# Kernel optimization log

Hardware: AMD Instinct MI355X
Metric: run time of the kernel (lower is better)

Reference implementation:

```python
import jax, jax.numpy as jnp
import numpy as np
import math

EMB_DIM = 2048
HEAD_NUMS = 16
HEAD_DIM = EMB_DIM // HEAD_NUMS


def setup_inputs() -> dict:
    key = jax.random.key(0)
    k1, k2, k3, k4, k5 = jax.random.split(key, 5)
    B, S = 2, 2048
    X = jax.random.normal(k1, (B, S, EMB_DIM), dtype=jnp.float32)
    mask = jnp.ones((B, S), dtype=jnp.int32)
    # torch nn.Linear weights: [out_features, in_features]
    W_qkv = jax.random.normal(k2, (3 * EMB_DIM, EMB_DIM), dtype=jnp.float32) / math.sqrt(EMB_DIM)
    b_qkv = jax.random.normal(k3, (3 * EMB_DIM,), dtype=jnp.float32) * 0.01
    W_o = jax.random.normal(k4, (EMB_DIM, EMB_DIM), dtype=jnp.float32) / math.sqrt(EMB_DIM)
    b_o = jax.random.normal(k5, (EMB_DIM,), dtype=jnp.float32) * 0.01
    return {"X": X, "mask": mask, "W_qkv": W_qkv, "b_qkv": b_qkv, "W_o": W_o, "b_o": b_o}


def _rope_tables(seq_len):
    # Bug-faithful to source: exponent divides by full emb_dim, not head_dim.
    angle = 1.0 / jnp.power(10000.0, jnp.arange(0, HEAD_DIM, 2, dtype=jnp.float32) / EMB_DIM)
    t = jnp.arange(seq_len, dtype=jnp.float32)
    freqs = t[:, None] * angle[None, :]            # [S, HEAD_DIM//2]
    freqs = jnp.repeat(freqs, 2, axis=-1)          # [S, HEAD_DIM] (repeat_interleave)
    return jnp.cos(freqs), jnp.sin(freqs)


def _trans(x):
    # de-interleave pairs, then concat([-odd, even]) along last dim (as in source)
    B, H, S, D = x.shape
    xr = x.reshape(B, H, S, D // 2, 2)
    x1, x2 = xr[..., 0], xr[..., 1]
    return jnp.concatenate([-x2, x1], axis=-1)


def reference(X, mask, W_qkv, b_qkv, W_o, b_o):
    B, S, E = X.shape
    cos, sin = _rope_tables(S)                      # [S, HEAD_DIM]
    qkv = X @ W_qkv.T + b_qkv                       # [B, S, 3E]
    qkv = qkv.reshape(B, S, 3, HEAD_NUMS, HEAD_DIM).transpose(2, 0, 3, 1, 4)
    Q, K, V = qkv[0], qkv[1], qkv[2]                # [B, H, S, D]
    c = cos[None, None, :, :]
    s = sin[None, None, :, :]
    Q = c * Q + s * _trans(Q)
    K = c * K + s * _trans(K)
    scores = jnp.einsum('bhqd,bhkd->bhqk', Q, K) / math.sqrt(HEAD_DIM)
    pad = mask[:, None, None, :]                    # [B,1,1,S]
    scores = jnp.where(pad == 0, -1e9, scores)
    attn = jax.nn.softmax(scores, axis=-1)          # dropout = identity (eval)
    out = jnp.einsum('bhqk,bhkd->bhqd', attn, V)    # [B,H,S,D]
    out = out.transpose(0, 2, 1, 3).reshape(B, S, E)
    return out @ W_o.T + b_o
```

## Files before the change

### kernel.cpp

```cpp
#include <hip/hip_runtime.h>
#include <hip/hip_bf16.h>
#include <math.h>

typedef __bf16 bf16x8 __attribute__((ext_vector_type(8)));
typedef float  f32x4  __attribute__((ext_vector_type(4)));
typedef float  f32x16 __attribute__((ext_vector_type(16)));
typedef unsigned short ushort_t;
typedef ushort_t us4 __attribute__((ext_vector_type(4)));

#define MFMA16(a, b, c) __builtin_amdgcn_mfma_f32_16x16x32_bf16((a), (b), (c), 0, 0, 0)
#define MFMA32(a, b, c) __builtin_amdgcn_mfma_f32_32x32x16_bf16((a), (b), (c), 0, 0, 0)

__device__ __forceinline__ float bf2f(ushort_t h) {
    union { unsigned u; float f; } v; v.u = ((unsigned)h) << 16; return v.f;
}
__device__ __forceinline__ ushort_t f2bf(float x) {
    union { float f; unsigned u; } v; v.f = x;
    unsigned r = v.u + 0x7FFFu + ((v.u >> 16) & 1u);
    return (ushort_t)(r >> 16);
}
__device__ __forceinline__ void gl2lds16(const void* g, void* l) {
    __builtin_amdgcn_global_load_lds((__attribute__((address_space(1))) void*)(g),
                                     (__attribute__((address_space(3))) void*)(l),
                                     16, 0, 0);
}

__global__ __launch_bounds__(256) void detect_kernel(const ushort_t* __restrict__ w, int* flag)
{
    __shared__ int cnt[256];
    const int t = threadIdx.x;
    int c = 0;
    for (int i = t; i < 65536; i += 256) {
        const unsigned hw = w[i];
        const unsigned e = (hw >> 7) & 0xFFu;
        if (e == 0xFFu || (e == 0u && (hw & 0x7Fu) != 0u)) c++;
    }
    cnt[t] = c;
    __syncthreads();
    for (int s = 128; s > 0; s >>= 1) {
        if (t < s) cnt[t] += cnt[t + s];
        __syncthreads();
    }
    if (t == 0) flag[0] = (cnt[0] >= 8) ? 1 : 0;
}

__global__ __launch_bounds__(256) void convert_kernel(const void* __restrict__ src,
                                                      ushort_t* __restrict__ dst,
                                                      int n, const int* __restrict__ flag)
{
    const int i0 = (blockIdx.x * 256 + threadIdx.x) * 8;
    if (i0 + 8 > n) return;
    if (flag[0]) {
        const f32x4 a = *(const f32x4*)((const float*)src + i0);
        const f32x4 b = *(const f32x4*)((const float*)src + i0 + 4);
        ushort_t o[8];
        o[0]=f2bf(a[0]); o[1]=f2bf(a[1]); o[2]=f2bf(a[2]); o[3]=f2bf(a[3]);
        o[4]=f2bf(b[0]); o[5]=f2bf(b[1]); o[6]=f2bf(b[2]); o[7]=f2bf(b[3]);
        *(bf16x8*)(dst + i0) = *(const bf16x8*)o;
    } else {
        *(bf16x8*)(dst + i0) = *(const bf16x8*)((const ushort_t*)src + i0);
    }
}

__global__ __launch_bounds__(512, 2) void gemm256_bt_bias(
    const ushort_t* __restrict__ A, const ushort_t* __restrict__ B,
    const ushort_t* __restrict__ bias, ushort_t* __restrict__ C,
    int M, int N, int K)
{
    __shared__ __align__(16) ushort_t SM[65536];
    const int tid = threadIdx.x;
    const int l = tid & 63, ln = l & 15, q2 = l >> 4;
    const int w = tid >> 6, wm = w >> 2, wn = w & 3;
    const int m0 = blockIdx.y * 256, n0 = blockIdx.x * 256;
    const int NT = K >> 6;

#define STG_A256(slot, kbase, o) do { \
    const int s_ = (o) * 512 + tid; const int r_ = s_ >> 2; \
    const int q_ = (s_ & 3) ^ ((r_ >> 1) & 3); \
    gl2lds16(A + (size_t)(m0 + r_) * K + (kbase) + q_ * 8, \
             SM + (slot) * 16384 + s_ * 8); } while (0)
#define STG_B256(slot, kbase, o) do { \
    const int s_ = (o) * 512 + tid; const int r_ = s_ >> 2; \
    const int q_ = (s_ & 3) ^ ((r_ >> 1) & 3); \
    gl2lds16(B + (size_t)(n0 + r_) * K + (kbase) + q_ * 8, \
             SM + (slot) * 16384 + 8192 + s_ * 8); } while (0)
#define DSA256(slot, row) (*(const bf16x8*)(SM + (slot) * 16384 + (row) * 32 + ((q2 ^ (((row) >> 1) & 3)) << 3)))
#define DSB256(slot, row) (*(const bf16x8*)(SM + (slot) * 16384 + 8192 + (row) * 32 + ((q2 ^ (((row) >> 1) & 3)) << 3)))
#define BAR256() asm volatile("s_barrier" ::: "memory")

    f32x4 acc[8][4];
    const f32x4 z4 = {0.f, 0.f, 0.f, 0.f};
#pragma unroll
    for (int i = 0; i < 8; i++)
#pragma unroll
        for (int j = 0; j < 4; j++) acc[i][j] = z4;

    STG_A256(0, 0, 0);  STG_A256(0, 0, 1);  STG_B256(0, 0, 0);  STG_B256(0, 0, 1);
    STG_A256(1, 32, 0); STG_A256(1, 32, 1); STG_B256(1, 32, 0); STG_B256(1, 32, 1);
    if (NT > 1) STG_A256(2, 64, 0);
    asm volatile("s_waitcnt vmcnt(5)" ::: "memory");
    BAR256();

    for (int t = 0; t < NT; ++t) {
        const int s0 = (2 * t) & 3, s1 = (2 * t + 1) & 3;
        const int sA = (2 * t + 2) & 3, sB = (2 * t + 3) & 3;
        const int kA = (t + 1) << 6, kB = kA + 32, kC = (t + 2) << 6;
        const bool stAB = (t < NT - 1), stC = (t < NT - 2);
        const int rA0 = wm * 128, rA1 = wm * 128 + 64, rB = wn * 64;
        bf16x8 a0[4], a1[4], b00[2], b01[2], b10[2], b11[2];

#pragma unroll
        for (int ii = 0; ii < 4; ii++) a0[ii] = DSA256(s0, rA0 + ii * 16 + ln);
        b00[0] = DSB256(s0, rB + ln);
        b00[1] = DSB256(s0, rB + 16 + ln);
        if (stAB) STG_A256(sA, kA, 1);
        __builtin_amdgcn_s_setprio(1);
#pragma unroll
        for (int ii = 0; ii < 4; ii++) {
            acc[ii][0] = MFMA16(a0[ii], b00[0], acc[ii][0]);
            acc[ii][1] = MFMA16(a0[ii], b00[1], acc[ii][1]);
        }
        __builtin_amdgcn_s_setprio(0);
        if (stAB) { asm volatile("s_waitcnt vmcnt(2)" ::: "memory"); }
        else      { asm volatile("s_waitcnt vmcnt(0)" ::: "memory"); }
        BAR256();

#pragma unroll
        for (int ii = 0; ii < 4; ii++) a1[ii] = DSA256(s1, rA0 + ii * 16 + ln);
        b01[0] = DSB256(s1, rB + ln);
        b01[1] = DSB256(s1, rB + 16 + ln);
        if (stAB) STG_B256(sA, kA, 0);
        __builtin_amdgcn_s_setprio(1);
#pragma unroll
        for (int ii = 0; ii < 4; ii++) {
            acc[ii][0] = MFMA16(a1[ii], b01[0], acc[ii][0]);
            acc[ii][1] = MFMA16(a1[ii], b01[1], acc[ii][1]);
        }
        __builtin_amdgcn_s_setprio(0);
        BAR256();

        b10[0] = DSB256(s0, rB + 32 + ln);
        b10[1] = DSB256(s0, rB + 48 + ln);
        if (stAB) STG_B256(sA, kA, 1);
        __builtin_amdgcn_s_setprio(1);
#pragma unroll
        for (int ii = 0; ii < 4; ii++) {
            acc[ii][2] = MFMA16(a0[ii], b10[0], acc[ii][2]);
            acc[ii][3] = MFMA16(a0[ii], b10[1], acc[ii][3]);
        }
        __builtin_amdgcn_s_setprio(0);
        BAR256();

        b11[0] = DSB256(s1, rB + 32 + ln);
        b11[1] = DSB256(s1, rB + 48 + ln);
        if (stAB) STG_A256(sB, kB, 0);
        __builtin_amdgcn_s_setprio(1);
#pragma unroll
        for (int ii = 0; ii < 4; ii++) {
            acc[ii][2] = MFMA16(a1[ii], b11[0], acc[ii][2]);
            acc[ii][3] = MFMA16(a1[ii], b11[1], acc[ii][3]);
        }
        __builtin_amdgcn_s_setprio(0);
        BAR256();

#pragma unroll
        for (int ii = 0; ii < 4; ii++) a0[ii] = DSA256(s0, rA1 + ii * 16 + ln);
        if (stAB) STG_A256(sB, kB, 1);
        __builtin_amdgcn_s_setprio(1);
#pragma unroll
        for (int ii = 0; ii < 4; ii++) {
            acc[4 + ii][2] = MFMA16(a0[ii], b10[0], acc[4 + ii][2]);
            acc[4 + ii][3] = MFMA16(a0[ii], b10[1], acc[4 + ii][3]);
        }
        __builtin_amdgcn_s_setprio(0);
        BAR256();

#pragma unroll
        for (int ii = 0; ii < 4; ii++) a1[ii] = DSA256(s1, rA1 + ii * 16 + ln);
        if (stAB) STG_B256(sB, kB, 0);
        __builtin_amdgcn_s_setprio(1);
#pragma unroll
        for (int ii = 0; ii < 4; ii++) {
            acc[4 + ii][2] = MFMA16(a1[ii], b11[0], acc[4 + ii][2]);
            acc[4 + ii][3] = MFMA16(a1[ii], b11[1], acc[4 + ii][3]);
        }
        __builtin_amdgcn_s_setprio(0);
        BAR256();

        if (stAB) STG_B256(sB, kB, 1);
        __builtin_amdgcn_s_setprio(1);
#pragma unroll
        for (int ii = 0; ii < 4; ii++) {
            acc[4 + ii][0] = MFMA16(a0[ii], b00[0], acc[4 + ii][0]);
            acc[4 + ii][1] = MFMA16(a0[ii], b00[1], acc[4 + ii][1]);
        }
        __builtin_amdgcn_s_setprio(0);
        BAR256();

        if (stC) STG_A256(s0, kC, 0);
        __builtin_amdgcn_s_setprio(1);
#pragma unroll
        for (int ii = 0; ii < 4; ii++) {
            acc[4 + ii][0] = MFMA16(a1[ii], b01[0], acc[4 + ii][0]);
            acc[4 + ii][1] = MFMA16(a1[ii], b01[1], acc[4 + ii][1]);
        }
        __builtin_amdgcn_s_setprio(0);
        if (t < NT - 2)       { asm volatile("s_waitcnt vmcnt(5)" ::: "memory"); }
        else if (t == NT - 2) { asm volatile("s_waitcnt vmcnt(4)" ::: "memory"); }
        BAR256();
    }

#pragma unroll
    for (int j = 0; j < 4; j++) {
        const int n = n0 + wn * 64 + j * 16 + ln;
        const float bv = bf2f(bias[n]);
#pragma unroll
        for (int i = 0; i < 8; i++) {
            const int mrow = m0 + wm * 128 + i * 16 + q2 * 4;
#pragma unroll
            for (int r = 0; r < 4; r++)
                C[(size_t)(mrow + r) * N + n] = f2bf(acc[i][j][r] + bv);
        }
    }
#undef STG_A256
#undef STG_B256
#undef DSA256
#undef DSB256
#undef BAR256
}

__global__ __launch_bounds__(256) void gemm_bt_bias_out(
    const ushort_t* __restrict__ A, const ushort_t* __restrict__ B,
    const ushort_t* __restrict__ bias, void* __restrict__ C,
    int M, int N, int K, const int* __restrict__ flag)
{
    __shared__ __align__(16) ushort_t As[128 * 32];
    __shared__ __align__(16) ushort_t Bs[128 * 32];
    const int tid = threadIdx.x;
    const int w = tid >> 6, l = tid & 63, q = l >> 4, ln = l & 15;
    const int wm = w >> 1, wn = w & 1;
    const int m0 = blockIdx.y * 128, n0 = blockIdx.x * 128;
    const int sr = tid >> 2;
    const int sc = (tid & 3) * 8;

    f32x4 acc[4][4];
    const f32x4 z4 = {0.f, 0.f, 0.f, 0.f};
    for (int i = 0; i < 4; i++) for (int j = 0; j < 4; j++) acc[i][j] = z4;

    for (int k0 = 0; k0 < K; k0 += 32) {
        __syncthreads();
        gl2lds16(A + (size_t)(m0 + sr) * K + k0 + sc,       As + sr * 32 + sc);
        gl2lds16(A + (size_t)(m0 + 64 + sr) * K + k0 + sc,  As + (64 + sr) * 32 + sc);
        gl2lds16(B + (size_t)(n0 + sr) * K + k0 + sc,       Bs + sr * 32 + sc);
        gl2lds16(B + (size_t)(n0 + 64 + sr) * K + k0 + sc,  Bs + (64 + sr) * 32 + sc);
        __syncthreads();
        bf16x8 a[4], bb[4];
        for (int i = 0; i < 4; i++)
            a[i]  = *(const bf16x8*)(As + (wm * 64 + i * 16 + ln) * 32 + q * 8);
        for (int j = 0; j < 4; j++)
            bb[j] = *(const bf16x8*)(Bs + (wn * 64 + j * 16 + ln) * 32 + q * 8);
        for (int i = 0; i < 4; i++)
            for (int j = 0; j < 4; j++)
                acc[i][j] = MFMA16(a[i], bb[j], acc[i][j]);
    }
    const int f = flag[0];
    for (int j = 0; j < 4; j++) {
        const int n = n0 + wn * 64 + j * 16 + ln;
        const float bv = bf2f(bias[n]);
        for (int i = 0; i < 4; i++) {
            const int mrow = m0 + wm * 64 + i * 16 + q * 4;
            for (int r = 0; r < 4; r++) {
                const float val = acc[i][j][r] + bv;
                const size_t idx = (size_t)(mrow + r) * N + n;
                if (f) ((float*)C)[idx] = val;
                else   ((ushort_t*)C)[idx] = f2bf(val);
            }
        }
    }
}

__global__ __launch_bounds__(256) void rope_kernel(ushort_t* qkv)
{
    const int bs = blockIdx.x;
    const int s = bs & 2047;
    const int t = threadIdx.x;
    const size_t base = (size_t)bs * 6144;
    float cv[8], sv[8], qa[8], qp[8], ka[8], kp[8];
    for (int u = 0; u < 8; u++) {
        const int e = u * 256 + t;
        const int j = e & 127;
        const int p = (j < 64) ? (2 * j + 1) : (2 * (j - 64));
        const int hb = e - j;
        const float ang = powf(10000.0f, -(float)(2 * (j >> 1)) / 2048.0f);
        sincosf((float)s * ang, &sv[u], &cv[u]);
        qa[u] = bf2f(qkv[base + hb + j]);
        qp[u] = bf2f(qkv[base + hb + p]);
        ka[u] = bf2f(qkv[base + 2048 + hb + j]);
        kp[u] = bf2f(qkv[base + 2048 + hb + p]);
    }
    __syncthreads();
    for (int u = 0; u < 8; u++) {
        const int e = u * 256 + t;
        const int j = e & 127;
        const int hb = e - j;
        const float sg = (j < 64) ? -1.0f : 1.0f;
        qkv[base + hb + j]        = f2bf(cv[u] * qa[u] + sv[u] * sg * qp[u]);
        qkv[base + 2048 + hb + j] = f2bf(cv[u] * ka[u] + sv[u] * sg * kp[u]);
    }
}

__global__ __launch_bounds__(256) void vtrans_kernel(const ushort_t* __restrict__ qkv,
                                                     ushort_t* __restrict__ Vt)
{
    __shared__ ushort_t tile[64][130];
    const int blk = blockIdx.x;
    const int st = blk & 31, h = (blk >> 5) & 15, b = blk >> 9;
    const int t = threadIdx.x;
    for (int i = 0; i < 32; i++) {
        const int e = i * 256 + t;
        const int r = e >> 7, c = e & 127;
        tile[r][c] = qkv[(size_t)(b * 2048 + st * 64 + r) * 6144 + 4096 + h * 128 + c];
    }
    __syncthreads();
    const int d = t >> 1, s0 = (t & 1) * 32;
    const size_t obase = ((size_t)(b * 16 + h) * 128 + d) * 2048 + st * 64 + s0;
    for (int k = 0; k < 32; k++)
        Vt[obase + k] = tile[s0 + k][d];
}

__global__ __launch_bounds__(256) void flash_kernel(
    const ushort_t* __restrict__ qkv, const ushort_t* __restrict__ Vt,
    const int* __restrict__ mask, ushort_t* __restrict__ AO)
{
    __shared__ __align__(16) ushort_t Ks[64 * 136];
    __shared__ __align__(16) ushort_t Vs[128 * 136];
    __shared__ __align__(16) ushort_t Ps[4 * 32 * 72];
    const int t = threadIdx.x;
    const int w = t >> 6, l = t & 63, lq = l & 31, q2 = l >> 5;
    const int qb = blockIdx.x * 128, h = blockIdx.y, b = blockIdx.z;
    const size_t brow = (size_t)b * 2048;
    const float scale = 0.08838834764831845f;
    const int qrow = qb + w * 32 + lq;

    bf16x8 qf[8];
#pragma unroll
    for (int kb = 0; kb < 8; kb++)
        qf[kb] = *(const bf16x8*)(qkv + (brow + qrow) * 6144 + h * 128 + kb * 16 + q2 * 8);

    float m_old = -1e30f, lsum = 0.f;
    f32x16 acc_o[4];
#pragma unroll
    for (int dt = 0; dt < 4; dt++)
#pragma unroll
        for (int r = 0; r < 16; r++) acc_o[dt][r] = 0.f;

    for (int s0 = 0; s0 < 2048; s0 += 64) {
        const int mk = mask[brow + s0 + l];
        const unsigned long long bm = __ballot(mk != 0);
        __syncthreads();
#pragma unroll
        for (int i = 0; i < 4; i++) {
            const int c = i * 256 + t;
            const int row = c >> 4, cb = c & 15;
            *(bf16x8*)(Ks + row * 136 + cb * 8) =
                *(const bf16x8*)(qkv + (brow + s0 + row) * 6144 + 2048 + h * 128 + cb * 8);
        }
#pragma unroll
        for (int i = 0; i < 4; i++) {
            const int c = i * 256 + t;
            const int row = c >> 3, cb = c & 7;
            *(bf16x8*)(Vs + row * 136 + cb * 8) =
                *(const bf16x8*)(Vt + ((size_t)(b * 16 + h) * 128 + row) * 2048 + s0 + cb * 8);
        }
        __syncthreads();
        f32x16 sa[2];
#pragma unroll
        for (int mt = 0; mt < 2; mt++) {
#pragma unroll
            for (int r = 0; r < 16; r++) sa[mt][r] = 0.f;
#pragma unroll
            for (int kb = 0; kb < 8; kb++) {
                bf16x8 a = *(const bf16x8*)(Ks + (mt * 32 + lq) * 136 + kb * 16 + q2 * 8);
                sa[mt] = MFMA32(a, qf[kb], sa[mt]);
            }
        }
        float p[32];
        float mr = -1e30f;
#pragma unroll
        for (int mt = 0; mt < 2; mt++)
#pragma unroll
            for (int r = 0; r < 16; r++) {
                const int srow = mt * 32 + (r & 3) + 8 * (r >> 2) + 4 * q2;
                const float bias = ((bm >> srow) & 1ull) ? 0.f : -1e9f;
                const float v = sa[mt][r] * scale + bias;
                p[mt * 16 + r] = v;
                mr = fmaxf(mr, v);
            }
        mr = fmaxf(mr, __shfl_xor(mr, 32, 64));
        const float mnew = fmaxf(m_old, mr);
        const float alpha = __expf(m_old - mnew);
        float rs = 0.f;
#pragma unroll
        for (int i = 0; i < 32; i++) { p[i] = __expf(p[i] - mnew); rs += p[i]; }
        rs += __shfl_xor(rs, 32, 64);
        lsum = alpha * lsum + rs;
        m_old = mnew;
#pragma unroll
        for (int dt = 0; dt < 4; dt++)
#pragma unroll
            for (int r = 0; r < 16; r++) acc_o[dt][r] *= alpha;
#pragma unroll
        for (int mt = 0; mt < 2; mt++)
#pragma unroll
            for (int r2 = 0; r2 < 4; r2++) {
                us4 pk;
#pragma unroll
                for (int j = 0; j < 4; j++) pk[j] = f2bf(p[mt * 16 + r2 * 4 + j]);
                *(us4*)(Ps + (w * 32 + lq) * 72 + mt * 32 + r2 * 8 + q2 * 4) = pk;
            }
        bf16x8 pf[4];
#pragma unroll
        for (int kb = 0; kb < 4; kb++)
            pf[kb] = *(const bf16x8*)(Ps + (w * 32 + lq) * 72 + kb * 16 + q2 * 8);
#pragma unroll
        for (int dt = 0; dt < 4; dt++)
#pragma unroll
            for (int kb = 0; kb < 4; kb++) {
                bf16x8 va = *(const bf16x8*)(Vs + (dt * 32 + lq) * 136 + kb * 16 + q2 * 8);
                acc_o[dt] = MFMA32(va, pf[kb], acc_o[dt]);
            }
    }
    __syncthreads();
    const float inv = (lsum > 0.f) ? 1.0f / lsum : 0.f;
#pragma unroll
    for (int dt = 0; dt < 4; dt++)
#pragma unroll
        for (int r2 = 0; r2 < 4; r2++) {
            us4 ov;
#pragma unroll
            for (int j = 0; j < 4; j++) ov[j] = f2bf(acc_o[dt][r2 * 4 + j] * inv);
            *(us4*)(Vs + (w * 32 + lq) * 136 + dt * 32 + r2 * 8 + q2 * 4) = ov;
        }
#pragma unroll
    for (int i = 0; i < 8; i++) {
        const int row = i * 4 + (l >> 4), ch = l & 15;
        bf16x8 vv = *(const bf16x8*)(Vs + (w * 32 + row) * 136 + ch * 8);
        *(bf16x8*)(AO + (brow + qb + w * 32 + row) * 2048 + h * 128 + ch * 8) = vv;
    }
}

extern "C" void kernel_launch(void* const* d_in, const int* in_sizes, int n_in,
                              void* d_out, int out_size, void* d_ws, size_t ws_size,
                              hipStream_t stream)
{
    (void)in_sizes; (void)n_in; (void)out_size; (void)ws_size;
    const void* X    = d_in[0];
    const int*  mask = (const int*)d_in[1];
    const void* Wqkv = d_in[2];
    const void* bqkv = d_in[3];
    const void* Wo   = d_in[4];
    const void* bo   = d_in[5];

    int*      flag  = (int*)d_ws;
    ushort_t* Xc    = (ushort_t*)d_ws + 16;
    ushort_t* Wqkvc = Xc + 8388608;
    ushort_t* bqkvc = Wqkvc + 12582912;
    ushort_t* Woc   = bqkvc + 6144;
    ushort_t* boc   = Woc + 4194304;
    ushort_t* qkv   = boc + 2048;
    ushort_t* Vt    = Wqkvc;
    ushort_t* AO    = Xc;

    detect_kernel<<<1, 256, 0, stream>>>((const ushort_t*)Wqkv, flag);
    convert_kernel<<<4096, 256, 0, stream>>>(X,    Xc,    8388608,  flag);
    convert_kernel<<<6144, 256, 0, stream>>>(Wqkv, Wqkvc, 12582912, flag);
    convert_kernel<<<3,    256, 0, stream>>>(bqkv, bqkvc, 6144,     flag);
    convert_kernel<<<2048, 256, 0, stream>>>(Wo,   Woc,   4194304,  flag);
    convert_kernel<<<1,    256, 0, stream>>>(bo,   boc,   2048,     flag);

    gemm256_bt_bias<<<dim3(6144 / 256, 4096 / 256), 512, 0, stream>>>(Xc, Wqkvc, bqkvc, qkv, 4096, 6144, 2048);
    rope_kernel<<<4096, 256, 0, stream>>>(qkv);
    vtrans_kernel<<<1024, 256, 0, stream>>>(qkv, Vt);
    flash_kernel<<<dim3(16, 16, 2), 256, 0, stream>>>(qkv, Vt, mask, AO);
    gemm_bt_bias_out<<<dim3(2048 / 128, 4096 / 128), 256, 0, stream>>>(AO, Woc, boc, d_out, 4096, 2048, 2048, flag);
}
```

Measured before the change: 608.9 us.

## Register-prefetch K/V tiles, swizzle LDS, keep P in registers in flash kernel

The flash attention kernel now prefetches the next K and V tiles into registers while the current tile is being computed. Shared memory uses an XOR swizzle instead of padded rows, which shrinks LDS enough to target two blocks per CU. The P matrix no longer round-trips through LDS; it is packed with cvt_pk_bf16 and rearranged with permlane32_swap. Further changes skip the mask math for fully unmasked tiles, only rescale the accumulator when the running max grows by more than a threshold, and raise wave priority around MFMA blocks. These changes add register pressure, and the lazy rescale lets exponentials exceed 1 within a bounded range.

```diff
diff --git a/kernel.cpp b/kernel.cpp
--- a/kernel.cpp
+++ b/kernel.cpp
@@ -328,19 +328,20 @@
         Vt[obase + k] = tile[s0 + k][d];
 }
 
-__global__ __launch_bounds__(256) void flash_kernel(
+__global__ __launch_bounds__(256, 2) void flash_kernel(
     const ushort_t* __restrict__ qkv, const ushort_t* __restrict__ Vt,
     const int* __restrict__ mask, ushort_t* __restrict__ AO)
 {
-    __shared__ __align__(16) ushort_t Ks[64 * 136];
-    __shared__ __align__(16) ushort_t Vs[128 * 136];
-    __shared__ __align__(16) ushort_t Ps[4 * 32 * 72];
+    __shared__ __align__(16) ushort_t SM[16384];
+    ushort_t* Ks = SM;
+    ushort_t* Vs = SM + 8192;
     const int t = threadIdx.x;
     const int w = t >> 6, l = t & 63, lq = l & 31, q2 = l >> 5;
     const int qb = blockIdx.x * 128, h = blockIdx.y, b = blockIdx.z;
     const size_t brow = (size_t)b * 2048;
     const float scale = 0.08838834764831845f;
     const int qrow = qb + w * 32 + lq;
+    const size_t vbase = (size_t)(b * 16 + h) * 128;
 
     bf16x8 qf[8];
 #pragma unroll
@@ -353,82 +354,124 @@
     for (int dt = 0; dt < 4; dt++)
 #pragma unroll
         for (int r = 0; r < 16; r++) acc_o[dt][r] = 0.f;
+
+    bf16x8 kst[4], vst[4];
+#pragma unroll
+    for (int i = 0; i < 4; i++) {
+        const int s_ = i * 256 + t; const int row = s_ >> 4; const int u = s_ & 15;
+        kst[i] = *(const bf16x8*)(qkv + (brow + row) * 6144 + 2048 + h * 128 + u * 8);
+    }
+#pragma unroll
+    for (int i = 0; i < 4; i++) {
+        const int s_ = i * 256 + t; const int row = s_ >> 3; const int u = s_ & 7;
+        vst[i] = *(const bf16x8*)(Vt + (vbase + row) * 2048 + u * 8);
+    }
 
     for (int s0 = 0; s0 < 2048; s0 += 64) {
         const int mk = mask[brow + s0 + l];
         const unsigned long long bm = __ballot(mk != 0);
-        __syncthreads();
+        asm volatile("s_waitcnt lgkmcnt(0)" ::: "memory");
+        asm volatile("s_barrier" ::: "memory");
 #pragma unroll
         for (int i = 0; i < 4; i++) {
-            const int c = i * 256 + t;
-            const int row = c >> 4, cb = c & 15;
-            *(bf16x8*)(Ks + row * 136 + cb * 8) =
-                *(const bf16x8*)(qkv + (brow + s0 + row) * 6144 + 2048 + h * 128 + cb * 8);
+            const int s_ = i * 256 + t; const int row = s_ >> 4; const int u = s_ & 15;
+            *(bf16x8*)(Ks + row * 128 + ((u ^ (row & 15)) << 3)) = kst[i];
         }
 #pragma unroll
         for (int i = 0; i < 4; i++) {
-            const int c = i * 256 + t;
-            const int row = c >> 3, cb = c & 7;
-            *(bf16x8*)(Vs + row * 136 + cb * 8) =
-                *(const bf16x8*)(Vt + ((size_t)(b * 16 + h) * 128 + row) * 2048 + s0 + cb * 8);
-        }
-        __syncthreads();
+            const int s_ = i * 256 + t; const int row = s_ >> 3; const int u = s_ & 7;
+            *(bf16x8*)(Vs + row * 64 + ((u ^ (row & 7)) << 3)) = vst[i];
+        }
+        if (s0 + 64 < 2048) {
+#pragma unroll
+            for (int i = 0; i < 4; i++) {
+                const int s_ = i * 256 + t; const int row = s_ >> 4; const int u = s_ & 15;
+                kst[i] = *(const bf16x8*)(qkv + (brow + s0 + 64 + row) * 6144 + 2048 + h * 128 + u * 8);
+            }
+#pragma unroll
+            for (int i = 0; i < 4; i++) {
+                const int s_ = i * 256 + t; const int row = s_ >> 3; const int u = s_ & 7;
+                vst[i] = *(const bf16x8*)(Vt + (vbase + row) * 2048 + s0 + 64 + u * 8);
+            }
+        }
+        asm volatile("s_waitcnt lgkmcnt(0)" ::: "memory");
+        asm volatile("s_barrier" ::: "memory");
+
         f32x16 sa[2];
 #pragma unroll
         for (int mt = 0; mt < 2; mt++) {
 #pragma unroll
             for (int r = 0; r < 16; r++) sa[mt][r] = 0.f;
+            const int row = mt * 32 + lq;
+            __builtin_amdgcn_s_setprio(1);
 #pragma unroll
             for (int kb = 0; kb < 8; kb++) {
-                bf16x8 a = *(const bf16x8*)(Ks + (mt * 32 + lq) * 136 + kb * 16 + q2 * 8);
+                bf16x8 a = *(const bf16x8*)(Ks + row * 128 + (((kb * 2 + q2) ^ (row & 15)) << 3));
                 sa[mt] = MFMA32(a, qf[kb], sa[mt]);
             }
+            __builtin_amdgcn_s_setprio(0);
         }
         float p[32];
         float mr = -1e30f;
-#pragma unroll
-        for (int mt = 0; mt < 2; mt++)
-#pragma unroll
-            for (int r = 0; r < 16; r++) {
-                const int srow = mt * 32 + (r & 3) + 8 * (r >> 2) + 4 * q2;
-                const float bias = ((bm >> srow) & 1ull) ? 0.f : -1e9f;
-                const float v = sa[mt][r] * scale + bias;
-                p[mt * 16 + r] = v;
-                mr = fmaxf(mr, v);
+        if (bm == ~0ull) {
+#pragma unroll
+            for (int mt = 0; mt < 2; mt++)
+#pragma unroll
+                for (int r = 0; r < 16; r++) {
+                    const float v = sa[mt][r] * scale;
+                    p[mt * 16 + r] = v;
+                    mr = fmaxf(mr, v);
+                }
+        } else {
+#pragma unroll
+            for (int mt = 0; mt < 2; mt++)
+#pragma unroll
+                for (int r = 0; r < 16; r++) {
+                    const int srow = mt * 32 + (r & 3) + 8 * (r >> 2) + 4 * q2;
+                    const float bias = ((bm >> srow) & 1ull) ? 0.f : -1e9f;
+                    const float v = sa[mt][r] * scale + bias;
+                    p[mt * 16 + r] = v;
+                    mr = fmaxf(mr, v);
+                }
+        }
+        mr = fmaxf(mr, __shfl_xor(mr, 32, 64));
+        if (!__all(mr <= m_old + 8.0f)) {
+            const float mnew = fmaxf(m_old, mr);
+            const float alpha = __expf(m_old - mnew);
+            lsum *= alpha;
+#pragma unroll
+            for (int dt = 0; dt < 4; dt++)
+#pragma unroll
+                for (int r = 0; r < 16; r++) acc_o[dt][r] *= alpha;
+            m_old = mnew;
+        }
+        float rs = 0.f;
+#pragma unroll
+        for (int i = 0; i < 32; i++) { p[i] = __expf(p[i] - m_old); rs += p[i]; }
+        rs += __shfl_xor(rs, 32, 64);
+        lsum += rs;
+
+#pragma unroll
+        for (int kb = 0; kb < 4; kb++) {
+            const int bb = (kb >> 1) * 16 + (kb & 1) * 8;
+            unsigned w01, w23, w45, w67;
+            asm("v_cvt_pk_bf16_f32 %0, %1, %2" : "=v"(w01) : "v"(p[bb + 0]), "v"(p[bb + 1]));
+            asm("v_cvt_pk_bf16_f32 %0, %1, %2" : "=v"(w23) : "v"(p[bb + 2]), "v"(p[bb + 3]));
+            asm("v_cvt_pk_bf16_f32 %0, %1, %2" : "=v"(w45) : "v"(p[bb + 4]), "v"(p[bb + 5]));
+            asm("v_cvt_pk_bf16_f32 %0, %1, %2" : "=v"(w67) : "v"(p[bb + 6]), "v"(p[bb + 7]));
+            asm("v_permlane32_swap_b32 %0, %1" : "+v"(w01), "+v"(w45));
+            asm("v_permlane32_swap_b32 %0, %1" : "+v"(w23), "+v"(w67));
+            union { unsigned u[4]; bf16x8 v8; } pu;
+            pu.u[0] = w01; pu.u[1] = w23; pu.u[2] = w45; pu.u[3] = w67;
+            __builtin_amdgcn_s_setprio(1);
+#pragma unroll
+            for (int dt = 0; dt < 4; dt++) {
+                const int row = dt * 32 + lq;
+                bf16x8 va = *(const bf16x8*)(Vs + row * 64 + (((kb * 2 + q2) ^ (row & 7)) << 3));
+                acc_o[dt] = MFMA32(va, pu.v8, acc_o[dt]);
             }
-        mr = fmaxf(mr, __shfl_xor(mr, 32, 64));
-        const float mnew = fmaxf(m_old, mr);
-        const float alpha = __expf(m_old - mnew);
-        float rs = 0.f;
-#pragma unroll
-        for (int i = 0; i < 32; i++) { p[i] = __expf(p[i] - mnew); rs += p[i]; }
-        rs += __shfl_xor(rs, 32, 64);
-        lsum = alpha * lsum + rs;
-        m_old = mnew;
-#pragma unroll
-        for (int dt = 0; dt < 4; dt++)
-#pragma unroll
-            for (int r = 0; r < 16; r++) acc_o[dt][r] *= alpha;
-#pragma unroll
-        for (int mt = 0; mt < 2; mt++)
-#pragma unroll
-            for (int r2 = 0; r2 < 4; r2++) {
-                us4 pk;
-#pragma unroll
-                for (int j = 0; j < 4; j++) pk[j] = f2bf(p[mt * 16 + r2 * 4 + j]);
-                *(us4*)(Ps + (w * 32 + lq) * 72 + mt * 32 + r2 * 8 + q2 * 4) = pk;
-            }
-        bf16x8 pf[4];
-#pragma unroll
-        for (int kb = 0; kb < 4; kb++)
-            pf[kb] = *(const bf16x8*)(Ps + (w * 32 + lq) * 72 + kb * 16 + q2 * 8);
-#pragma unroll
-        for (int dt = 0; dt < 4; dt++)
-#pragma unroll
-            for (int kb = 0; kb < 4; kb++) {
-                bf16x8 va = *(const bf16x8*)(Vs + (dt * 32 + lq) * 136 + kb * 16 + q2 * 8);
-                acc_o[dt] = MFMA32(va, pf[kb], acc_o[dt]);
-            }
+            __builtin_amdgcn_s_setprio(0);
+        }
     }
     __syncthreads();
     const float inv = (lsum > 0.f) ? 1.0f / lsum : 0.f;
@@ -439,13 +482,17 @@
             us4 ov;
 #pragma unroll
             for (int j = 0; j < 4; j++) ov[j] = f2bf(acc_o[dt][r2 * 4 + j] * inv);
-            *(us4*)(Vs + (w * 32 + lq) * 136 + dt * 32 + r2 * 8 + q2 * 4) = ov;
-        }
+            const int row = w * 32 + lq;
+            const int unit = dt * 4 + r2;
+            *(us4*)(SM + row * 128 + ((unit ^ (row & 15)) << 3) + q2 * 4) = ov;
+        }
+    __syncthreads();
 #pragma unroll
     for (int i = 0; i < 8; i++) {
-        const int row = i * 4 + (l >> 4), ch = l & 15;
-        bf16x8 vv = *(const bf16x8*)(Vs + (w * 32 + row) * 136 + ch * 8);
-        *(bf16x8*)(AO + (brow + qb + w * 32 + row) * 2048 + h * 128 + ch * 8) = vv;
+        const int rl = i * 4 + (l >> 4), ch = l & 15;
+        const int row = w * 32 + rl;
+        bf16x8 vv = *(const bf16x8*)(SM + row * 128 + ((ch ^ (row & 15)) << 3));
+        *(bf16x8*)(AO + (brow + qb + row) * 2048 + h * 128 + ch * 8) = vv;
     }
 }
 
```

Result: faster. 578.9 us (-4.9%).
